# Kernel optimization log

Hardware: AMD Instinct MI355X
Metric: run time of the kernel (lower is better)

## Reference

```python
import jax, jax.numpy as jnp
import numpy as np


def setup_inputs() -> dict:
    key = jax.random.key(0)
    ks = jax.random.split(key, 7)
    B, T, E, H = 256, 512, 256, 256
    s = 1.0 / np.sqrt(E + H)
    return {
        "embedding": jax.random.normal(ks[0], (B, T, E), dtype=jnp.float32),
        "Wz": jax.random.normal(ks[1], (H, E + H), dtype=jnp.float32) * s,
        "bz": jax.random.normal(ks[2], (H,), dtype=jnp.float32) * s,
        "Wr": jax.random.normal(ks[3], (H, E + H), dtype=jnp.float32) * s,
        "br": jax.random.normal(ks[4], (H,), dtype=jnp.float32) * s,
        "Wm": jax.random.normal(ks[5], (H, E + H), dtype=jnp.float32) * s,
        "bm": jax.random.normal(ks[6], (H,), dtype=jnp.float32) * s,
    }


def reference(embedding, Wz, bz, Wr, br, Wm, bm):
    # embedding: [B, T, E] -> time-major [T, B, E] (matches Encoder.forward transpose)
    emb = jnp.transpose(embedding, (1, 0, 2))
    B = emb.shape[1]
    H = Wz.shape[0]
    h0 = jnp.zeros((B, H), dtype=embedding.dtype)

    def step(h, x):  # x: [B, E], h: [B, H]
        xi = jnp.concatenate([x, h], axis=1)            # [B, E+H]
        z = jax.nn.sigmoid(xi @ Wz.T + bz)              # update gate
        r = jax.nn.sigmoid(xi @ Wr.T + br)              # reset gate
        xm = jnp.concatenate([x, r * h], axis=1)
        h_cand = jnp.tanh(xm @ Wm.T + bm)
        h_new = (1.0 - z) * h + z * h_cand
        return h_new, h_new

    _, hs = jax.lax.scan(step, h0, emb)                 # hs: [T, B, H]
    return jnp.transpose(hs, (1, 0, 2))                 # [B, T, H]
```

## Files before the change

kernel.cpp:

```cpp
#include <hip/hip_runtime.h>

typedef _Float16 half8_t __attribute__((ext_vector_type(8)));
typedef _Float16 half2_t __attribute__((ext_vector_type(2)));
typedef float floatx4 __attribute__((ext_vector_type(4)));

#define B_DIM 256
#define T_DIM 512
#define E_DIM 256
#define H_DIM 256
#define MROWS (B_DIM * T_DIM)

__device__ __forceinline__ half2_t mk2(_Float16 x, _Float16 y) {
    half2_t v; v[0] = x; v[1] = y; return v;
}

__device__ __forceinline__ float fdot2f(half2_t a, half2_t b, float c) {
#if __has_builtin(__builtin_amdgcn_fdot2)
    return __builtin_amdgcn_fdot2(a, b, c, false);
#else
    return c + (float)a[0] * (float)b[0] + (float)a[1] * (float)b[1];
#endif
}

__global__ __launch_bounds__(256, 2) void gemm_x(
    const float* __restrict__ emb,
    const float* __restrict__ Wz, const float* __restrict__ bz,
    const float* __restrict__ Wr, const float* __restrict__ br,
    const float* __restrict__ Wm, const float* __restrict__ bm,
    _Float16* __restrict__ Xz, _Float16* __restrict__ Xr,
    float* __restrict__ Xm)
{
    const int n0 = blockIdx.x * 128;
    const int m0 = blockIdx.y * 128;
    const int gate = n0 >> 8;
    const int ng0 = n0 & 255;
    const float* W    = (gate == 0) ? Wz : (gate == 1) ? Wr : Wm;
    const float* bias = (gate == 0) ? bz : (gate == 1) ? br : bm;

    __shared__ __align__(16) _Float16 lA[128 * 40];
    __shared__ __align__(16) _Float16 lB[128 * 40];

    const int t = threadIdx.x;
    const int lane = t & 63;
    const int wave = t >> 6;
    const int wm = (wave >> 1) * 64;
    const int wn = (wave & 1) * 64;
    const int lq = lane >> 4;
    const int lr = lane & 15;

    floatx4 acc[4][4];
    #pragma unroll
    for (int i = 0; i < 4; ++i)
        #pragma unroll
        for (int j = 0; j < 4; ++j)
            acc[i][j] = (floatx4)0.0f;

    const int srow = t >> 1;
    const int scol = (t & 1) * 16;
    const float* aSrc = emb + (size_t)(m0 + srow) * E_DIM + scol;
    const float* bSrc = W + (size_t)(ng0 + srow) * (E_DIM + H_DIM) + scol;

    for (int k0 = 0; k0 < E_DIM; k0 += 32) {
        float ta[16], tb[16];
        #pragma unroll
        for (int u = 0; u < 4; ++u) {
            *(float4*)(ta + 4 * u) = *(const float4*)(aSrc + k0 + 4 * u);
            *(float4*)(tb + 4 * u) = *(const float4*)(bSrc + k0 + 4 * u);
        }
        half8_t a0, a1, b0, b1;
        #pragma unroll
        for (int u = 0; u < 8; ++u) {
            a0[u] = (_Float16)ta[u]; a1[u] = (_Float16)ta[u + 8];
            b0[u] = (_Float16)tb[u]; b1[u] = (_Float16)tb[u + 8];
        }
        __syncthreads();
        *(half8_t*)&lA[srow * 40 + scol]     = a0;
        *(half8_t*)&lA[srow * 40 + scol + 8] = a1;
        *(half8_t*)&lB[srow * 40 + scol]     = b0;
        *(half8_t*)&lB[srow * 40 + scol + 8] = b1;
        __syncthreads();

        half8_t af[4], bf[4];
        #pragma unroll
        for (int i = 0; i < 4; ++i)
            af[i] = *(const half8_t*)&lA[(wm + i * 16 + lr) * 40 + lq * 8];
        #pragma unroll
        for (int j = 0; j < 4; ++j)
            bf[j] = *(const half8_t*)&lB[(wn + j * 16 + lr) * 40 + lq * 8];
        #pragma unroll
        for (int i = 0; i < 4; ++i)
            #pragma unroll
            for (int j = 0; j < 4; ++j)
                acc[i][j] = __builtin_amdgcn_mfma_f32_16x16x32_f16(
                    af[i], bf[j], acc[i][j], 0, 0, 0);
    }

    if (gate < 2) {
        _Float16* dst = (gate == 0) ? Xz : Xr;
        #pragma unroll
        for (int j = 0; j < 4; ++j) {
            const int ng = ng0 + wn + j * 16 + lr;
            const float bv = bias[ng];
            #pragma unroll
            for (int i = 0; i < 4; ++i) {
                const int mrow = m0 + wm + i * 16 + lq * 4;
                #pragma unroll
                for (int r = 0; r < 4; ++r)
                    dst[(size_t)(mrow + r) * H_DIM + ng] =
                        (_Float16)(acc[i][j][r] + bv);
            }
        }
    } else {
        #pragma unroll
        for (int j = 0; j < 4; ++j) {
            const int ng = ng0 + wn + j * 16 + lr;
            const float bv = bias[ng];
            #pragma unroll
            for (int i = 0; i < 4; ++i) {
                const int mrow = m0 + wm + i * 16 + lq * 4;
                #pragma unroll
                for (int r = 0; r < 4; ++r)
                    Xm[(size_t)(mrow + r) * H_DIM + ng] = acc[i][j][r] + bv;
            }
        }
    }
}

__global__ __launch_bounds__(512, 2) void gru_rec(
    const float* __restrict__ Wz,
    const float* __restrict__ Wr,
    const float* __restrict__ Wm,
    const _Float16* __restrict__ Xz,
    const _Float16* __restrict__ Xr,
    float* __restrict__ out)
{
    const int b = blockIdx.x;
    const int t = threadIdx.x;
    const int jA = t & 255;
    const int jB = t >> 1;
    const int hB = t & 1;

    __shared__ __align__(16) _Float16 hh[256];
    __shared__ float hf[256];
    __shared__ __align__(16) _Float16 rh[256];
    __shared__ float zl[256];

    half2_t w1[128];
    {
        const float* wrow = ((t < 256) ? Wz : Wr) + (size_t)jA * 512 + 256;
        #pragma unroll
        for (int k = 0; k < 64; ++k) {
            float4 f = ((const float4*)wrow)[k];
            w1[2 * k]     = mk2((_Float16)f.x, (_Float16)f.y);
            w1[2 * k + 1] = mk2((_Float16)f.z, (_Float16)f.w);
        }
    }
    half2_t w2[64];
    {
        const float* wrow = Wm + (size_t)jB * 512 + 256 + hB * 128;
        #pragma unroll
        for (int k = 0; k < 32; ++k) {
            float4 f = ((const float4*)wrow)[k];
            w2[2 * k]     = mk2((_Float16)f.x, (_Float16)f.y);
            w2[2 * k + 1] = mk2((_Float16)f.z, (_Float16)f.w);
        }
    }

    if (t < 256) { hh[t] = (_Float16)0.0f; hf[t] = 0.0f; }
    __syncthreads();

    const size_t rowbase = (size_t)b * T_DIM * H_DIM;
    float xa_n = (t < 256) ? (float)Xz[rowbase + jA] : (float)Xr[rowbase + jA];
    float xm_n = (hB == 0) ? out[rowbase + jB] : 0.0f;

    for (int ts = 0; ts < T_DIM; ++ts) {
        const float xa = xa_n;
        const float xm = xm_n;
        if (ts + 1 < T_DIM) {
            const size_t nb = rowbase + (size_t)(ts + 1) * H_DIM;
            xa_n = (t < 256) ? (float)Xz[nb + jA] : (float)Xr[nb + jA];
            xm_n = (hB == 0) ? out[nb + jB] : 0.0f;
        }

        float a0 = xa, a1 = 0.f, a2 = 0.f, a3 = 0.f;
        const half8_t* hp8 = (const half8_t*)hh;
        #pragma unroll
        for (int k = 0; k < 32; ++k) {
            half8_t hv = hp8[k];
            a0 = fdot2f(w1[4 * k],     mk2(hv[0], hv[1]), a0);
            a1 = fdot2f(w1[4 * k + 1], mk2(hv[2], hv[3]), a1);
            a2 = fdot2f(w1[4 * k + 2], mk2(hv[4], hv[5]), a2);
            a3 = fdot2f(w1[4 * k + 3], mk2(hv[6], hv[7]), a3);
        }
        const float a = (a0 + a1) + (a2 + a3);
        const float g = 1.0f / (1.0f + __expf(-a));
        if (t < 256) zl[jA] = g;
        else         rh[jA] = (_Float16)(g * hf[jA]);
        __syncthreads();

        float c0 = 0.f, c1 = 0.f;
        const half8_t* rp8 = (const half8_t*)(rh + hB * 128);
        #pragma unroll
        for (int k = 0; k < 16; ++k) {
            half8_t rv = rp8[k];
            c0 = fdot2f(w2[4 * k],     mk2(rv[0], rv[1]), c0);
            c1 = fdot2f(w2[4 * k + 1], mk2(rv[2], rv[3]), c1);
            c0 = fdot2f(w2[4 * k + 2], mk2(rv[4], rv[5]), c0);
            c1 = fdot2f(w2[4 * k + 3], mk2(rv[6], rv[7]), c1);
        }
        float c = c0 + c1;
        c += __shfl_xor(c, 1);
        if (hB == 0) {
            const float am = c + xm;
            const float hcand = 2.0f / (1.0f + __expf(-2.0f * am)) - 1.0f;
            const float z = zl[jB];
            const float hn = (1.0f - z) * hf[jB] + z * hcand;
            out[rowbase + (size_t)ts * H_DIM + jB] = hn;
            hf[jB] = hn;
            hh[jB] = (_Float16)hn;
        }
        __syncthreads();
    }
}

extern "C" void kernel_launch(void* const* d_in, const int* in_sizes, int n_in,
                              void* d_out, int out_size, void* d_ws, size_t ws_size,
                              hipStream_t stream) {
    (void)in_sizes; (void)n_in; (void)out_size; (void)ws_size;
    const float* emb = (const float*)d_in[0];
    const float* Wz  = (const float*)d_in[1];
    const float* bz  = (const float*)d_in[2];
    const float* Wr  = (const float*)d_in[3];
    const float* br  = (const float*)d_in[4];
    const float* Wm  = (const float*)d_in[5];
    const float* bm  = (const float*)d_in[6];
    float* out = (float*)d_out;

    _Float16* Xz = (_Float16*)d_ws;
    _Float16* Xr = Xz + (size_t)MROWS * H_DIM;

    dim3 g1(6, MROWS / 128);
    gemm_x<<<g1, 256, 0, stream>>>(emb, Wz, bz, Wr, br, Wm, bm, Xz, Xr, out);
    gru_rec<<<B_DIM, 512, 0, stream>>>(Wz, Wr, Wm, Xz, Xr, out);
}
```

Baseline: 1.191 ms.

## Restructure GRU recurrence into 4-lane k-split groups with register-held state

Rewrites the recurrent kernel so each group of 4 lanes splits the K dimension of two hidden rows across all three gates. Partial sums are reduced with DPP lane swaps, and h and z stay in registers instead of shared memory. LDS reads are XOR-swizzled to avoid bank conflicts, and the sigmoid and tanh now use a fast reciprocal. Occupancy is set to 1 block per CU and each thread now holds 192 packed weight registers, which risks register pressure or spills.

```diff
diff --git a/kernel.cpp b/kernel.cpp
--- a/kernel.cpp
+++ b/kernel.cpp
@@ -10,8 +10,8 @@
 #define H_DIM 256
 #define MROWS (B_DIM * T_DIM)
 
-__device__ __forceinline__ half2_t mk2(_Float16 x, _Float16 y) {
-    half2_t v; v[0] = x; v[1] = y; return v;
+__device__ __forceinline__ half2_t cvt2(float x, float y) {
+    half2_t v; v[0] = (_Float16)x; v[1] = (_Float16)y; return v;
 }
 
 __device__ __forceinline__ float fdot2f(half2_t a, half2_t b, float c) {
@@ -19,6 +19,33 @@
     return __builtin_amdgcn_fdot2(a, b, c, false);
 #else
     return c + (float)a[0] * (float)b[0] + (float)a[1] * (float)b[1];
+#endif
+}
+
+__device__ __forceinline__ float dpp_xor1(float x) {
+#if __has_builtin(__builtin_amdgcn_mov_dpp)
+    int i = __builtin_bit_cast(int, x);
+    i = __builtin_amdgcn_mov_dpp(i, 0xB1, 0xF, 0xF, true);
+    return __builtin_bit_cast(float, i);
+#else
+    return __shfl_xor(x, 1);
+#endif
+}
+__device__ __forceinline__ float dpp_xor2(float x) {
+#if __has_builtin(__builtin_amdgcn_mov_dpp)
+    int i = __builtin_bit_cast(int, x);
+    i = __builtin_amdgcn_mov_dpp(i, 0x4E, 0xF, 0xF, true);
+    return __builtin_bit_cast(float, i);
+#else
+    return __shfl_xor(x, 2);
+#endif
+}
+
+__device__ __forceinline__ float fast_rcp(float x) {
+#if __has_builtin(__builtin_amdgcn_rcpf)
+    return __builtin_amdgcn_rcpf(x);
+#else
+    return 1.0f / x;
 #endif
 }
 
@@ -126,7 +153,7 @@
     }
 }
 
-__global__ __launch_bounds__(512, 2) void gru_rec(
+__global__ __launch_bounds__(512, 1) void gru_rec(
     const float* __restrict__ Wz,
     const float* __restrict__ Wr,
     const float* __restrict__ Wm,
@@ -136,88 +163,126 @@
 {
     const int b = blockIdx.x;
     const int t = threadIdx.x;
-    const int jA = t & 255;
-    const int jB = t >> 1;
-    const int hB = t & 1;
+    const int g = t >> 2;
+    const int s = t & 3;
+    const int rowA = g;
+    const int rowB = g + 128;
+    const int col = g + ((s & 2) << 6);
 
     __shared__ __align__(16) _Float16 hh[256];
-    __shared__ float hf[256];
     __shared__ __align__(16) _Float16 rh[256];
-    __shared__ float zl[256];
-
-    half2_t w1[128];
+
+    half2_t wzA[32], wzB[32], wrA[32], wrB[32], wmA[32], wmB[32];
     {
-        const float* wrow = ((t < 256) ? Wz : Wr) + (size_t)jA * 512 + 256;
-        #pragma unroll
-        for (int k = 0; k < 64; ++k) {
-            float4 f = ((const float4*)wrow)[k];
-            w1[2 * k]     = mk2((_Float16)f.x, (_Float16)f.y);
-            w1[2 * k + 1] = mk2((_Float16)f.z, (_Float16)f.w);
+        const size_t sb = 256 + 64 * s;
+        const float4* pzA = (const float4*)(Wz + (size_t)rowA * 512 + sb);
+        const float4* pzB = (const float4*)(Wz + (size_t)rowB * 512 + sb);
+        const float4* prA = (const float4*)(Wr + (size_t)rowA * 512 + sb);
+        const float4* prB = (const float4*)(Wr + (size_t)rowB * 512 + sb);
+        const float4* pmA = (const float4*)(Wm + (size_t)rowA * 512 + sb);
+        const float4* pmB = (const float4*)(Wm + (size_t)rowB * 512 + sb);
+        #pragma unroll
+        for (int kk = 0; kk < 8; ++kk) {
+            const int lk = kk ^ (s << 1);
+            float4 f0, f1;
+            f0 = pzA[2*lk]; f1 = pzA[2*lk+1];
+            wzA[4*kk]=cvt2(f0.x,f0.y); wzA[4*kk+1]=cvt2(f0.z,f0.w);
+            wzA[4*kk+2]=cvt2(f1.x,f1.y); wzA[4*kk+3]=cvt2(f1.z,f1.w);
+            f0 = pzB[2*lk]; f1 = pzB[2*lk+1];
+            wzB[4*kk]=cvt2(f0.x,f0.y); wzB[4*kk+1]=cvt2(f0.z,f0.w);
+            wzB[4*kk+2]=cvt2(f1.x,f1.y); wzB[4*kk+3]=cvt2(f1.z,f1.w);
+            f0 = prA[2*lk]; f1 = prA[2*lk+1];
+            wrA[4*kk]=cvt2(f0.x,f0.y); wrA[4*kk+1]=cvt2(f0.z,f0.w);
+            wrA[4*kk+2]=cvt2(f1.x,f1.y); wrA[4*kk+3]=cvt2(f1.z,f1.w);
+            f0 = prB[2*lk]; f1 = prB[2*lk+1];
+            wrB[4*kk]=cvt2(f0.x,f0.y); wrB[4*kk+1]=cvt2(f0.z,f0.w);
+            wrB[4*kk+2]=cvt2(f1.x,f1.y); wrB[4*kk+3]=cvt2(f1.z,f1.w);
+            f0 = pmA[2*lk]; f1 = pmA[2*lk+1];
+            wmA[4*kk]=cvt2(f0.x,f0.y); wmA[4*kk+1]=cvt2(f0.z,f0.w);
+            wmA[4*kk+2]=cvt2(f1.x,f1.y); wmA[4*kk+3]=cvt2(f1.z,f1.w);
+            f0 = pmB[2*lk]; f1 = pmB[2*lk+1];
+            wmB[4*kk]=cvt2(f0.x,f0.y); wmB[4*kk+1]=cvt2(f0.z,f0.w);
+            wmB[4*kk+2]=cvt2(f1.x,f1.y); wmB[4*kk+3]=cvt2(f1.z,f1.w);
         }
     }
-    half2_t w2[64];
-    {
-        const float* wrow = Wm + (size_t)jB * 512 + 256 + hB * 128;
-        #pragma unroll
-        for (int k = 0; k < 32; ++k) {
-            float4 f = ((const float4*)wrow)[k];
-            w2[2 * k]     = mk2((_Float16)f.x, (_Float16)f.y);
-            w2[2 * k + 1] = mk2((_Float16)f.z, (_Float16)f.w);
-        }
-    }
-
-    if (t < 256) { hh[t] = (_Float16)0.0f; hf[t] = 0.0f; }
+
+    if (t < 256) hh[t] = (_Float16)0.0f;
     __syncthreads();
 
+    const char* hbase = (const char*)hh + s * 128;
+    const char* rbase = (const char*)rh + s * 128;
+
     const size_t rowbase = (size_t)b * T_DIM * H_DIM;
-    float xa_n = (t < 256) ? (float)Xz[rowbase + jA] : (float)Xr[rowbase + jA];
-    float xm_n = (hB == 0) ? out[rowbase + jB] : 0.0f;
-
+    const _Float16* xgp = (s & 1) ? Xr : Xz;
+
+    float hown = 0.0f;
+    float zown = 0.0f;
+
+    float xg_n = (float)xgp[rowbase + col];
+    float xm_n = (s & 1) ? 0.0f : out[rowbase + col];
+
+    #pragma unroll 1
     for (int ts = 0; ts < T_DIM; ++ts) {
-        const float xa = xa_n;
+        const float xg = xg_n;
         const float xm = xm_n;
         if (ts + 1 < T_DIM) {
             const size_t nb = rowbase + (size_t)(ts + 1) * H_DIM;
-            xa_n = (t < 256) ? (float)Xz[nb + jA] : (float)Xr[nb + jA];
-            xm_n = (hB == 0) ? out[nb + jB] : 0.0f;
-        }
-
-        float a0 = xa, a1 = 0.f, a2 = 0.f, a3 = 0.f;
-        const half8_t* hp8 = (const half8_t*)hh;
-        #pragma unroll
-        for (int k = 0; k < 32; ++k) {
-            half8_t hv = hp8[k];
-            a0 = fdot2f(w1[4 * k],     mk2(hv[0], hv[1]), a0);
-            a1 = fdot2f(w1[4 * k + 1], mk2(hv[2], hv[3]), a1);
-            a2 = fdot2f(w1[4 * k + 2], mk2(hv[4], hv[5]), a2);
-            a3 = fdot2f(w1[4 * k + 3], mk2(hv[6], hv[7]), a3);
-        }
-        const float a = (a0 + a1) + (a2 + a3);
-        const float g = 1.0f / (1.0f + __expf(-a));
-        if (t < 256) zl[jA] = g;
-        else         rh[jA] = (_Float16)(g * hf[jA]);
+            xg_n = (float)xgp[nb + col];
+            xm_n = (s & 1) ? 0.0f : out[nb + col];
+        }
+
+        float az = 0.f, ar = 0.f, zb = 0.f, rb = 0.f;
+        #pragma unroll
+        for (int kk = 0; kk < 8; ++kk) {
+            half8_t hv = *(const half8_t*)(hbase + ((kk * 16) ^ (s * 32)));
+            half2_t p0 = __builtin_shufflevector(hv, hv, 0, 1);
+            half2_t p1 = __builtin_shufflevector(hv, hv, 2, 3);
+            half2_t p2 = __builtin_shufflevector(hv, hv, 4, 5);
+            half2_t p3 = __builtin_shufflevector(hv, hv, 6, 7);
+            az = fdot2f(wzA[4*kk],   p0, az); az = fdot2f(wzA[4*kk+1], p1, az);
+            az = fdot2f(wzA[4*kk+2], p2, az); az = fdot2f(wzA[4*kk+3], p3, az);
+            ar = fdot2f(wrA[4*kk],   p0, ar); ar = fdot2f(wrA[4*kk+1], p1, ar);
+            ar = fdot2f(wrA[4*kk+2], p2, ar); ar = fdot2f(wrA[4*kk+3], p3, ar);
+            zb = fdot2f(wzB[4*kk],   p0, zb); zb = fdot2f(wzB[4*kk+1], p1, zb);
+            zb = fdot2f(wzB[4*kk+2], p2, zb); zb = fdot2f(wzB[4*kk+3], p3, zb);
+            rb = fdot2f(wrB[4*kk],   p0, rb); rb = fdot2f(wrB[4*kk+1], p1, rb);
+            rb = fdot2f(wrB[4*kk+2], p2, rb); rb = fdot2f(wrB[4*kk+3], p3, rb);
+        }
+        az += dpp_xor1(az); az += dpp_xor2(az);
+        ar += dpp_xor1(ar); ar += dpp_xor2(ar);
+        zb += dpp_xor1(zb); zb += dpp_xor2(zb);
+        rb += dpp_xor1(rb); rb += dpp_xor2(rb);
+        const float d01 = (s & 1) ? ar : az;
+        const float d23 = (s & 1) ? rb : zb;
+        const float dsum = (s & 2) ? d23 : d01;
+        const float gate = fast_rcp(1.0f + __expf(-(dsum + xg)));
+        const float hpair = dpp_xor1(hown);
+        if (s & 1) rh[col] = (_Float16)(gate * hpair);
+        else       zown = gate;
         __syncthreads();
 
-        float c0 = 0.f, c1 = 0.f;
-        const half8_t* rp8 = (const half8_t*)(rh + hB * 128);
-        #pragma unroll
-        for (int k = 0; k < 16; ++k) {
-            half8_t rv = rp8[k];
-            c0 = fdot2f(w2[4 * k],     mk2(rv[0], rv[1]), c0);
-            c1 = fdot2f(w2[4 * k + 1], mk2(rv[2], rv[3]), c1);
-            c0 = fdot2f(w2[4 * k + 2], mk2(rv[4], rv[5]), c0);
-            c1 = fdot2f(w2[4 * k + 3], mk2(rv[6], rv[7]), c1);
-        }
-        float c = c0 + c1;
-        c += __shfl_xor(c, 1);
-        if (hB == 0) {
-            const float am = c + xm;
-            const float hcand = 2.0f / (1.0f + __expf(-2.0f * am)) - 1.0f;
-            const float z = zl[jB];
-            const float hn = (1.0f - z) * hf[jB] + z * hcand;
-            out[rowbase + (size_t)ts * H_DIM + jB] = hn;
-            hf[jB] = hn;
-            hh[jB] = (_Float16)hn;
+        float ca = 0.f, cb = 0.f;
+        #pragma unroll
+        for (int kk = 0; kk < 8; ++kk) {
+            half8_t rv = *(const half8_t*)(rbase + ((kk * 16) ^ (s * 32)));
+            half2_t p0 = __builtin_shufflevector(rv, rv, 0, 1);
+            half2_t p1 = __builtin_shufflevector(rv, rv, 2, 3);
+            half2_t p2 = __builtin_shufflevector(rv, rv, 4, 5);
+            half2_t p3 = __builtin_shufflevector(rv, rv, 6, 7);
+            ca = fdot2f(wmA[4*kk],   p0, ca); ca = fdot2f(wmA[4*kk+1], p1, ca);
+            ca = fdot2f(wmA[4*kk+2], p2, ca); ca = fdot2f(wmA[4*kk+3], p3, ca);
+            cb = fdot2f(wmB[4*kk],   p0, cb); cb = fdot2f(wmB[4*kk+1], p1, cb);
+            cb = fdot2f(wmB[4*kk+2], p2, cb); cb = fdot2f(wmB[4*kk+3], p3, cb);
+        }
+        ca += dpp_xor1(ca); ca += dpp_xor2(ca);
+        cb += dpp_xor1(cb); cb += dpp_xor2(cb);
+        if (!(s & 1)) {
+            const float am = ((s & 2) ? cb : ca) + xm;
+            const float hcand = 1.0f - 2.0f * fast_rcp(1.0f + __expf(2.0f * am));
+            const float hn = (1.0f - zown) * hown + zown * hcand;
+            out[rowbase + (size_t)ts * H_DIM + col] = hn;
+            hown = hn;
+            hh[col] = (_Float16)hn;
         }
         __syncthreads();
     }
```

After: 1.268 ms. +6.5%, slower.
